# Optimization experiments

Measured on AMD Instinct MI355X. Metric: run time of the kernel, lower is better.

The kernel has to match this reference:

```python
import jax, jax.numpy as jnp
import numpy as np

B, T, N, F = 4, 12, 768, 32
H, K, KT, L = 64, 2, 3, 2
E = 24576
EPS = 1e-5


def setup_inputs() -> dict:
    key = jax.random.key(0)
    ks = iter(jax.random.split(key, 32))
    nrm = lambda shp, s=0.05: jax.random.normal(next(ks), shp, jnp.float32) * s
    inp = dict(
        x=jax.random.normal(next(ks), (B, T, N, F), jnp.float32),
        edge_index=jax.random.randint(next(ks), (2, E), 0, N),
        edge_weight=jax.random.uniform(next(ks), (E,), jnp.float32),
        in_proj_w=nrm((F, H)), in_proj_b=jnp.zeros((H,), jnp.float32),
        tc_w=nrm((L, 2, 3, H, H, KT)),           # [layer, tconv1/2, P/Q/R, out, in, k]
        tc_b=jnp.zeros((L, 2, 3, H), jnp.float32),
        cheb_w=nrm((L, K, H, H)), cheb_b=jnp.zeros((L, H), jnp.float32),
        bn_g=jnp.ones((L, N), jnp.float32), bn_b=jnp.zeros((L, N), jnp.float32),
        ln_g=jnp.ones((L, H), jnp.float32), ln_b=jnp.zeros((L, H), jnp.float32),
        out1_w=nrm((2 * H, H // 2)), out1_b=jnp.zeros((H // 2,), jnp.float32),
        oln_g=jnp.ones((H // 2,), jnp.float32), oln_b=jnp.zeros((H // 2,), jnp.float32),
        out2_w=nrm((H // 2, 1)), out2_b=jnp.zeros((1,), jnp.float32),
    )
    return inp


def _tconv(x, w, b):
    # gated temporal conv (GLU-style), 'same' padding along T. x: [B,T,N,C]
    xt = x.transpose(0, 3, 2, 1)  # [B,C,N,T]
    pad = (KT - 1) // 2
    def c(i):
        y = jax.lax.conv_general_dilated(
            xt, w[i][:, :, None, :], (1, 1), ((0, 0), (pad, pad)),
            dimension_numbers=('NCHW', 'OIHW', 'NCHW'))
        return y + b[i][None, :, None, None]
    out = jax.nn.relu(c(0) * jax.nn.sigmoid(c(1)) + c(2))
    return out.transpose(0, 3, 2, 1)


def _cheb(x, row, col, lap_w, theta, bias):
    # ChebConv with lambda_max=2: L_hat = -D^-1/2 A D^-1/2. x: [B,T,N,C]
    def lhat(z):
        zn = z.transpose(2, 0, 1, 3)                      # [N,B,T,C]
        msg = zn[col] * lap_w[:, None, None, None]        # gather source nodes
        agg = jax.ops.segment_sum(msg, row, num_segments=N)
        return agg.transpose(1, 2, 0, 3)
    tx0 = x
    out = jnp.einsum('btnc,cd->btnd', tx0, theta[0])
    if K > 1:
        tx1 = lhat(tx0)
        out = out + jnp.einsum('btnc,cd->btnd', tx1, theta[1])
        for k in range(2, K):
            tx2 = 2.0 * lhat(tx1) - tx0
            out = out + jnp.einsum('btnc,cd->btnd', tx2, theta[k])
            tx0, tx1 = tx1, tx2
    return out + bias


def reference(x, edge_index, edge_weight, in_proj_w, in_proj_b, tc_w, tc_b,
              cheb_w, cheb_b, bn_g, bn_b, ln_g, ln_b,
              out1_w, out1_b, oln_g, oln_b, out2_w, out2_b):
    row, col = edge_index[0], edge_index[1]
    deg = jax.ops.segment_sum(edge_weight, row, num_segments=N)
    dinv = jnp.where(deg > 0, jax.lax.rsqrt(jnp.maximum(deg, 1e-12)), 0.0)
    lap_w = -dinv[row] * edge_weight * dinv[col]

    h = x @ in_proj_w + in_proj_b  # [B,T,N,H]
    for l in range(L):
        z = _tconv(h, tc_w[l, 0], tc_b[l, 0])
        z = jax.nn.relu(_cheb(z, row, col, lap_w, cheb_w[l], cheb_b[l]))
        z = _tconv(z, tc_w[l, 1], tc_b[l, 1])
        # BatchNorm2d with nodes as channels: stats over (B,T,C) per node
        mu = z.mean(axis=(0, 1, 3), keepdims=True)
        var = z.var(axis=(0, 1, 3), keepdims=True)
        z = (z - mu) * jax.lax.rsqrt(var + EPS)
        z = z * bn_g[l][None, None, :, None] + bn_b[l][None, None, :, None]
        # LayerNorm over feature dim
        m2 = z.mean(-1, keepdims=True)
        v2 = z.var(-1, keepdims=True)
        z = (z - m2) * jax.lax.rsqrt(v2 + EPS) * ln_g[l] + ln_b[l]
        h = h + z  # dropout = identity (eval)

    emb = h[:, -1]  # [B,N,H] last timestep
    # pairwise linear: cat([row_h, col_h]) @ W == row_h @ W[:H] + col_h @ W[H:]
    a = emb @ out1_w[:H]             # [B,N,H/2]
    c = emb @ out1_w[H:] + out1_b    # [B,N,H/2]
    p = jax.nn.relu(a[:, :, None, :] + c[:, None, :, :])  # [B,N,N,H/2]
    pm = p.mean(-1, keepdims=True)
    pv = p.var(-1, keepdims=True)
    p = (p - pm) * jax.lax.rsqrt(pv + EPS) * oln_g + oln_b
    logits = (p @ out2_w)[..., 0] + out2_b[0]
    return jax.nn.sigmoid(logits)  # [B,N,N]
```

## Files before the change

kernel.cpp:

```cpp
#include <hip/hip_runtime.h>
#include <math.h>

#define NODES 768
#define BB 4
#define TT 12
#define FF 32
#define HH 64
#define EE 24576
#define EPSV 1e-5f

typedef short bf16x8 __attribute__((ext_vector_type(8)));
typedef float f32x4  __attribute__((ext_vector_type(4)));

__device__ __forceinline__ unsigned short f2bf(float f) {
  union { float f; unsigned int u; } c; c.f = f;
  unsigned int u = c.u;
  unsigned int r = (u + 0x7FFFu + ((u >> 16) & 1u)) >> 16;
  return (unsigned short)r;
}

constexpr int OFF_DEG    = 0;
constexpr int OFF_CNT    = 768;
constexpr int OFF_ROWPTR = 1600;
constexpr int OFF_OFF    = 2432;
constexpr int OFF_COLS   = 3200;
constexpr int OFF_WSEW   = 27776;
constexpr int OFF_WT     = 52352;
constexpr int OFF_THT    = 199808;
constexpr int OFF_WIN    = 216192;
constexpr int OFF_GW     = 222336;
constexpr int OFF_H      = 222400;
constexpr int OFF_ZA     = 2581696;
constexpr int OFF_ZB     = 4940992;
constexpr int OFF_AGG    = 7300288;
constexpr int OFF_MU     = 9659584;
constexpr int OFF_RSTD   = 9660352;
constexpr int OFF_A      = 9661120;
constexpr int OFF_C      = 9759424;

__global__ void prep_kernel(const float* __restrict__ tc_w, const float* __restrict__ cheb_w,
                            const float* __restrict__ in_proj_w, const float* __restrict__ out1_w,
                            const float* __restrict__ oln_g, const float* __restrict__ oln_b,
                            const float* __restrict__ out2_w, float* __restrict__ ws) {
  int idx = blockIdx.x * 256 + threadIdx.x;
  if (idx < 147456) {
    int lj = idx / 36864; int r = idx % 36864;
    int ks = r / 6144;    int r2 = r % 6144;
    int nt = r2 / 512;    int r3 = r2 % 512;
    int l  = r3 >> 3;     int j  = r3 & 7;
    int k  = ks * 32 + ((l >> 4) << 3) + j;
    int kk = k >> 6;      int in = k & 63;
    int col = nt * 16 + (l & 15);
    int g = col >> 6;     int o  = col & 63;
    float v = tc_w[(((lj * 3 + g) * 64 + o) * 64 + in) * 3 + kk];
    ((unsigned short*)(ws + OFF_WT))[idx] = f2bf(v);
  }
  int idx2 = idx - 147456;
  if (idx2 >= 0 && idx2 < 16384) {
    int i = idx2 & 63; int t = idx2 >> 6;
    int o = t & 63; t >>= 6;
    int k = t & 1; int l = t >> 1;
    ws[OFF_THT + idx2] = cheb_w[((l*2 + k)*64 + i)*64 + o];
  }
  int idx3 = idx2 - 16384;
  if (idx3 >= 0 && idx3 < 2048) {
    int i = idx3 & 31; int o = idx3 >> 5;
    ws[OFF_WIN + idx3] = in_proj_w[i*64 + o];
  }
  int idx5 = idx3 - 2048;
  if (idx5 >= 0 && idx5 < 768) {
    ws[OFF_DEG + idx5] = 0.0f;
    ((int*)ws)[OFF_CNT + idx5] = 0;
  }
  int idx6 = idx5 - 768;
  if (idx6 == 0) {
    float S1 = 0.f, S2 = 0.f;
    for (int d = 0; d < 32; d++) {
      float gw = oln_g[d] * out2_w[d];
      ws[OFF_GW + d] = gw;
      S1 += gw;
      S2 += oln_b[d] * out2_w[d];
    }
    ws[OFF_GW + 32] = S1;
    ws[OFF_GW + 33] = S2;
  }
}

__global__ void count_kernel(const int* __restrict__ edge_index, const float* __restrict__ ew,
                             float* __restrict__ ws) {
  int e = blockIdx.x * 256 + threadIdx.x;
  if (e >= EE) return;
  int r = edge_index[e];
  atomicAdd(&ws[OFF_DEG + r], ew[e]);
  atomicAdd(&((int*)ws)[OFF_CNT + r], 1);
}

__global__ void scan_kernel(float* __restrict__ ws) {
  __shared__ int s[NODES];
  int t = threadIdx.x;
  int* counts = (int*)ws + OFF_CNT;
  int* rowptr = (int*)ws + OFF_ROWPTR;
  int* off    = (int*)ws + OFF_OFF;
  int c = counts[t];
  s[t] = c;
  __syncthreads();
  for (int d = 1; d < NODES; d <<= 1) {
    int v = (t >= d) ? s[t - d] : 0;
    __syncthreads();
    s[t] += v;
    __syncthreads();
  }
  rowptr[t + 1] = s[t];
  if (t == 0) rowptr[0] = 0;
  off[t] = s[t] - c;
}

__global__ void scatter_kernel(const int* __restrict__ edge_index, const float* __restrict__ ew,
                               float* __restrict__ ws) {
  int e = blockIdx.x * 256 + threadIdx.x;
  if (e >= EE) return;
  int r = edge_index[e];
  int c = edge_index[EE + e];
  float w = ew[e];
  float dr = ws[OFF_DEG + r], dc = ws[OFF_DEG + c];
  float dir = dr > 0.f ? rsqrtf(fmaxf(dr, 1e-12f)) : 0.f;
  float dic = dc > 0.f ? rsqrtf(fmaxf(dc, 1e-12f)) : 0.f;
  float lw = -dir * w * dic;
  int pos = atomicAdd(&((int*)ws)[OFF_OFF + r], 1);
  ((int*)ws)[OFF_COLS + pos] = c;
  ws[OFF_WSEW + pos] = lw;
}

__global__ __launch_bounds__(64) void inproj_kernel(const float* __restrict__ x,
                                                    const float* __restrict__ in_proj_b,
                                                    float* __restrict__ ws) {
  int bid = blockIdx.x;
  int r0 = (bid >> 2) << 6;
  int o0 = (bid & 3) << 4;
  int row = r0 + threadIdx.x;
  float xr[32];
  const float4* xp = (const float4*)(x + row * 32);
#pragma unroll
  for (int i = 0; i < 8; i++) {
    float4 v = xp[i];
    xr[4*i] = v.x; xr[4*i+1] = v.y; xr[4*i+2] = v.z; xr[4*i+3] = v.w;
  }
  const float* WT = ws + OFF_WIN;
  float* h = ws + OFF_H;
  float4 res[4];
  float* rf = (float*)res;
#pragma unroll
  for (int oo = 0; oo < 16; oo++) {
    int o = o0 + oo;
    float acc = in_proj_b[o];
#pragma unroll
    for (int i = 0; i < 32; i++) acc += xr[i] * WT[o * 32 + i];
    rf[oo] = acc;
  }
  float4* op = (float4*)(h + row * 64 + o0);
#pragma unroll
  for (int q = 0; q < 4; q++) op[q] = res[q];
}

__global__ __launch_bounds__(256) void tconv_kernel(const float* __restrict__ src,
                                                    float* __restrict__ dst,
                                                    const unsigned short* __restrict__ WB,
                                                    const float* __restrict__ bias) {
  __shared__ unsigned short zls[6656];
  __shared__ float cbuf[12 * 192];
  unsigned char* zb = (unsigned char*)zls;
  int tid = threadIdx.x;
  int lane = tid & 63;
  int w = tid >> 6;
  int P0 = blockIdx.x * 6;
  int b  = P0 / NODES;
  int n0 = P0 % NODES;

  bf16x8 bfr[6][3];
#pragma unroll
  for (int ks = 0; ks < 6; ks++) {
#pragma unroll
    for (int c = 0; c < 3; c++) {
      int nt = w * 3 + c;
      bfr[ks][c] = *(const bf16x8*)(WB + (((ks * 12 + nt) * 64 + lane) << 3));
    }
  }
  float B0 = bias[tid & 63];
  float B1 = bias[64 + (tid & 63)];
  float B2 = bias[128 + (tid & 63)];

  for (int e = tid; e < 768; e += 256) {
    int pl = e / 128; int rr = (e >> 6) & 1; int in = e & 63;
    int ts = rr ? 13 : 0;
    int off = pl * 1792 + ts * 128 + ((in * 2) ^ ((ts & 7) << 4));
    *(unsigned short*)(zb + off) = 0;
  }
  for (int e = tid; e < 4608; e += 256) {
    int t = e / 384; int r = e % 384; int pl = r >> 6; int in = r & 63;
    float v = src[((b * TT + t) * NODES + n0 + pl) * HH + in];
    int ts = t + 1;
    int off = pl * 1792 + ts * 128 + ((in * 2) ^ ((ts & 7) << 4));
    *(unsigned short*)(zb + off) = f2bf(v);
  }
  __syncthreads();

  int tb = (lane >> 4) << 2;
  int cc = lane & 15;
  for (int p = 0; p < 6; p++) {
    bf16x8 afr[6];
#pragma unroll
    for (int ks = 0; ks < 6; ks++) {
      int k0 = ks * 32 + ((lane >> 4) << 3);
      int kk = k0 >> 6; int in0 = k0 & 63;
      int ts = (lane & 15) + kk;
      int off = p * 1792 + ts * 128 + ((in0 * 2) ^ ((ts & 7) << 4));
      afr[ks] = *(const bf16x8*)(zb + off);
    }
    f32x4 a0 = {0.f, 0.f, 0.f, 0.f};
    f32x4 a1 = a0, a2 = a0;
#pragma unroll
    for (int ks = 0; ks < 6; ks++) {
      a0 = __builtin_amdgcn_mfma_f32_16x16x32_bf16(afr[ks], bfr[ks][0], a0, 0, 0, 0);
      a1 = __builtin_amdgcn_mfma_f32_16x16x32_bf16(afr[ks], bfr[ks][1], a1, 0, 0, 0);
      a2 = __builtin_amdgcn_mfma_f32_16x16x32_bf16(afr[ks], bfr[ks][2], a2, 0, 0, 0);
    }
    __syncthreads();
#pragma unroll
    for (int r = 0; r < 4; r++) {
      int t = tb + r;
      if (t < 12) {
        cbuf[t * 192 + (w * 3 + 0) * 16 + cc] = a0[r];
        cbuf[t * 192 + (w * 3 + 1) * 16 + cc] = a1[r];
        cbuf[t * 192 + (w * 3 + 2) * 16 + cc] = a2[r];
      }
    }
    __syncthreads();
    int o = tid & 63;
    int n = n0 + p;
#pragma unroll
    for (int m = 0; m < 3; m++) {
      int t = (tid >> 6) + (m << 2);
      float v0 = cbuf[t * 192 + o]       + B0;
      float v1 = cbuf[t * 192 + 64 + o]  + B1;
      float v2 = cbuf[t * 192 + 128 + o] + B2;
      float g = 1.f / (1.f + __expf(-v1));
      dst[((b * TT + t) * NODES + n) * HH + o] = fmaxf(v0 * g + v2, 0.f);
    }
  }
}

__global__ __launch_bounds__(256) void agg_kernel(const float* __restrict__ za,
                                                  float* __restrict__ agg,
                                                  const float* __restrict__ ws) {
  int n = blockIdx.x >> 1;
  int half = blockIdx.x & 1;
  const int* rowptr = (const int*)ws + OFF_ROWPTR;
  const int* cols = (const int*)ws + OFF_COLS;
  const float* wsrt = ws + OFF_WSEW;
  int e0 = rowptr[n], e1 = rowptr[n + 1];
  int tid = threadIdx.x;
  int hh = tid & 63;
  int bt0 = tid >> 6;
  float acc[6];
#pragma unroll
  for (int p = 0; p < 6; p++) acc[p] = 0.f;
  for (int e = e0; e < e1; e++) {
    int c = cols[e];
    float w = wsrt[e];
    const float* zp = za + c * HH + hh;
#pragma unroll
    for (int p = 0; p < 6; p++) {
      int bt = bt0 + (((half * 6) + p) << 2);
      acc[p] += w * zp[bt * NODES * HH];
    }
  }
#pragma unroll
  for (int p = 0; p < 6; p++) {
    int bt = bt0 + (((half * 6) + p) << 2);
    agg[(bt * NODES + n) * HH + hh] = acc[p];
  }
}

__global__ __launch_bounds__(64) void cheb_kernel(const float* __restrict__ za,
                                                  const float* __restrict__ agg,
                                                  float* __restrict__ zb,
                                                  const float* __restrict__ thetaT,
                                                  const float* __restrict__ bias) {
  int bid = blockIdx.x;
  int r0 = (bid >> 2) << 6;
  int o0 = (bid & 3) << 4;
  int row = r0 + threadIdx.x;
  float xz[64], xa[64];
  const float4* zp = (const float4*)(za + row * 64);
  const float4* ap = (const float4*)(agg + row * 64);
#pragma unroll
  for (int i = 0; i < 16; i++) {
    float4 v = zp[i];
    xz[4*i] = v.x; xz[4*i+1] = v.y; xz[4*i+2] = v.z; xz[4*i+3] = v.w;
    float4 w = ap[i];
    xa[4*i] = w.x; xa[4*i+1] = w.y; xa[4*i+2] = w.z; xa[4*i+3] = w.w;
  }
  float4 res[4];
  float* rf = (float*)res;
#pragma unroll
  for (int oo = 0; oo < 16; oo++) {
    int o = o0 + oo;
    float acc = bias[o];
    const float* t0 = thetaT + o * 64;
    const float* t1 = thetaT + 4096 + o * 64;
#pragma unroll
    for (int i = 0; i < 64; i++) acc += xz[i] * t0[i] + xa[i] * t1[i];
    rf[oo] = fmaxf(acc, 0.f);
  }
  float4* op = (float4*)(zb + row * 64 + o0);
#pragma unroll
  for (int q = 0; q < 4; q++) op[q] = res[q];
}

__global__ __launch_bounds__(256) void bnstat_kernel(const float* __restrict__ z,
                                                     float* __restrict__ mu,
                                                     float* __restrict__ rstd) {
  int n = blockIdx.x;
  int tid = threadIdx.x;
  float s = 0.f, ss = 0.f;
  for (int p = tid; p < 48 * 64; p += 256) {
    int bt = p >> 6, hh = p & 63;
    float v = z[(bt * NODES + n) * HH + hh];
    s += v; ss += v * v;
  }
  int wave = tid >> 6, lane = tid & 63;
#pragma unroll
  for (int d = 32; d >= 1; d >>= 1) { s += __shfl_down(s, d, 64); ss += __shfl_down(ss, d, 64); }
  __shared__ float rs[4], rss[4];
  if (lane == 0) { rs[wave] = s; rss[wave] = ss; }
  __syncthreads();
  if (tid == 0) {
    float S = 0.f, SS = 0.f;
    for (int w = 0; w < 4; w++) { S += rs[w]; SS += rss[w]; }
    float m = S / 3072.f;
    float var = SS / 3072.f - m * m;
    mu[n] = m;
    rstd[n] = rsqrtf(var + EPSV);
  }
}

__global__ __launch_bounds__(256) void bnln_kernel(const float* __restrict__ z,
                                                   float* __restrict__ h,
                                                   const float* __restrict__ mu,
                                                   const float* __restrict__ rstd,
                                                   const float* __restrict__ bn_g,
                                                   const float* __restrict__ bn_b,
                                                   const float* __restrict__ ln_g,
                                                   const float* __restrict__ ln_b) {
  int row = blockIdx.x * 4 + (threadIdx.x >> 6);
  int lane = threadIdx.x & 63;
  int n = row % NODES;
  float v = z[row * 64 + lane];
  v = (v - mu[n]) * rstd[n] * bn_g[n] + bn_b[n];
  float s = v, ss = v * v;
#pragma unroll
  for (int d = 32; d >= 1; d >>= 1) { s += __shfl_xor(s, d, 64); ss += __shfl_xor(ss, d, 64); }
  float m = s * (1.f / 64.f);
  float var = ss * (1.f / 64.f) - m * m;
  float r2 = rsqrtf(var + EPSV);
  v = (v - m) * r2 * ln_g[lane] + ln_b[lane];
  h[row * 64 + lane] += v;
}

__global__ __launch_bounds__(256) void proj_kernel(const float* __restrict__ out1_w,
                                                   const float* __restrict__ out1_b,
                                                   float* __restrict__ ws) {
  __shared__ float wl[128 * 32];
  __shared__ float rl[4][64];
  int r0 = blockIdx.x * 4;
  int tid = threadIdx.x;
  const float* h = ws + OFF_H;
  for (int p = tid; p < 4096; p += 256) wl[p] = out1_w[p];
  {
    int rr = tid >> 6, ii = tid & 63;
    int row = r0 + rr;
    int b = row / NODES, n = row % NODES;
    rl[rr][ii] = h[((b * TT + (TT - 1)) * NODES + n) * 64 + ii];
  }
  __syncthreads();
  int rr = tid >> 6;
  int o = tid & 63;
  int part = o >> 5, oc = o & 31;
  float acc = part ? out1_b[oc] : 0.f;
  const float* wcol = wl + part * 64 * 32;
#pragma unroll
  for (int i = 0; i < 64; i++) acc += rl[rr][i] * wcol[i * 32 + oc];
  int row = r0 + rr;
  if (part == 0) (ws + OFF_A)[row * 32 + oc] = acc;
  else           (ws + OFF_C)[row * 32 + oc] = acc;
}

__global__ __launch_bounds__(256) void pair_kernel(const float* __restrict__ ws,
                                                   const float* __restrict__ out2_b,
                                                   float* __restrict__ out) {
  __shared__ float al[16 * 33], cl[16 * 33], gwl[34];
  int bidx = blockIdx.x;
  int b = bidx / (48 * 48);
  int rem = bidx % (48 * 48);
  int i0 = (rem / 48) * 16;
  int j0 = (rem % 48) * 16;
  int tid = threadIdx.x;
  const float* abuf = ws + OFF_A;
  const float* cbuf = ws + OFF_C;
  if (tid < 34) gwl[tid] = ws[OFF_GW + tid];
  for (int p = tid; p < 512; p += 256) {
    int rr = p >> 5, dd = p & 31;
    al[rr * 33 + dd] = abuf[(b * NODES + i0 + rr) * 32 + dd];
    cl[rr * 33 + dd] = cbuf[(b * NODES + j0 + rr) * 32 + dd];
  }
  __syncthreads();
  int ti = tid >> 4;
  int tj = tid & 15;
  float s1 = 0.f, s2 = 0.f, sg = 0.f;
#pragma unroll
  for (int d = 0; d < 32; d++) {
    float v = al[ti * 33 + d] + cl[tj * 33 + d];
    v = fmaxf(v, 0.f);
    s1 += v; s2 += v * v; sg += v * gwl[d];
  }
  float m = s1 * (1.f / 32.f);
  float var = s2 * (1.f / 32.f) - m * m;
  float rstd = rsqrtf(var + EPSV);
  float logit = rstd * (sg - m * gwl[32]) + gwl[33] + out2_b[0];
  float sig = 1.f / (1.f + __expf(-logit));
  out[(b * NODES + (i0 + ti)) * NODES + (j0 + tj)] = sig;
}

extern "C" void kernel_launch(void* const* d_in, const int* in_sizes, int n_in,
                              void* d_out, int out_size, void* d_ws, size_t ws_size,
                              hipStream_t stream) {
  const float* x          = (const float*)d_in[0];
  const int*   edge_index = (const int*)d_in[1];
  const float* edge_weight= (const float*)d_in[2];
  const float* in_proj_w  = (const float*)d_in[3];
  const float* in_proj_b  = (const float*)d_in[4];
  const float* tc_w       = (const float*)d_in[5];
  const float* tc_b       = (const float*)d_in[6];
  const float* cheb_w     = (const float*)d_in[7];
  const float* cheb_b     = (const float*)d_in[8];
  const float* bn_g       = (const float*)d_in[9];
  const float* bn_b       = (const float*)d_in[10];
  const float* ln_g       = (const float*)d_in[11];
  const float* ln_b       = (const float*)d_in[12];
  const float* out1_w     = (const float*)d_in[13];
  const float* out1_b     = (const float*)d_in[14];
  const float* oln_g      = (const float*)d_in[15];
  const float* oln_b      = (const float*)d_in[16];
  const float* out2_w     = (const float*)d_in[17];
  const float* out2_b     = (const float*)d_in[18];
  float* ws  = (float*)d_ws;
  float* out = (float*)d_out;

  hipLaunchKernelGGL(prep_kernel, dim3(668), dim3(256), 0, stream,
                     tc_w, cheb_w, in_proj_w, out1_w, oln_g, oln_b, out2_w, ws);
  hipLaunchKernelGGL(count_kernel, dim3(96), dim3(256), 0, stream, edge_index, edge_weight, ws);
  hipLaunchKernelGGL(scan_kernel, dim3(1), dim3(768), 0, stream, ws);
  hipLaunchKernelGGL(scatter_kernel, dim3(96), dim3(256), 0, stream, edge_index, edge_weight, ws);
  hipLaunchKernelGGL(inproj_kernel, dim3(2304), dim3(64), 0, stream, x, in_proj_b, ws);

  float* h   = ws + OFF_H;
  float* za  = ws + OFF_ZA;
  float* zb  = ws + OFF_ZB;
  float* agg = ws + OFF_AGG;
  float* mu  = ws + OFF_MU;
  float* rstd= ws + OFF_RSTD;
  const unsigned short* WB = (const unsigned short*)(ws + OFF_WT);

  for (int l = 0; l < 2; l++) {
    hipLaunchKernelGGL(tconv_kernel, dim3(512), dim3(256), 0, stream,
                       h, za, WB + (l * 2 + 0) * 36864, tc_b + (l * 2 + 0) * 192);
    hipLaunchKernelGGL(agg_kernel, dim3(1536), dim3(256), 0, stream, za, agg, ws);
    hipLaunchKernelGGL(cheb_kernel, dim3(2304), dim3(64), 0, stream,
                       za, agg, zb, ws + OFF_THT + l * 8192, cheb_b + l * 64);
    hipLaunchKernelGGL(tconv_kernel, dim3(512), dim3(256), 0, stream,
                       zb, za, WB + (l * 2 + 1) * 36864, tc_b + (l * 2 + 1) * 192);
    hipLaunchKernelGGL(bnstat_kernel, dim3(768), dim3(256), 0, stream, za, mu, rstd);
    hipLaunchKernelGGL(bnln_kernel, dim3(9216), dim3(256), 0, stream,
                       za, h, mu, rstd, bn_g + l * NODES, bn_b + l * NODES,
                       ln_g + l * 64, ln_b + l * 64);
  }

  hipLaunchKernelGGL(proj_kernel, dim3(768), dim3(256), 0, stream, out1_w, out1_b, ws);
  hipLaunchKernelGGL(pair_kernel, dim3(9216), dim3(256), 0, stream, ws, out2_b, out);
}
```

Baseline: 330.4 us.

## Fuse graph preprocessing, halve tconv tile, fuse batchnorm stats with layernorm

Merges the count, scan and scatter kernels into one single-block kernel that keeps degrees and offsets in shared memory, removing two launches and the global atomics. Halves the nodes per tconv block (6 to 3), doubling the grid to 1024 blocks, and switches to float4 loads with packed bf16 stores. Fuses the batchnorm statistics and the BN+LN apply into one per-node kernel that caches the node slice in LDS, removing a second pass over z. The single-block graph kernel serializes 24K edges on one CU, and smaller tconv tiles reload the weights more often.

```diff
diff --git a/kernel.cpp b/kernel.cpp
--- a/kernel.cpp
+++ b/kernel.cpp
@@ -19,10 +19,7 @@
   return (unsigned short)r;
 }
 
-constexpr int OFF_DEG    = 0;
-constexpr int OFF_CNT    = 768;
 constexpr int OFF_ROWPTR = 1600;
-constexpr int OFF_OFF    = 2432;
 constexpr int OFF_COLS   = 3200;
 constexpr int OFF_WSEW   = 27776;
 constexpr int OFF_WT     = 52352;
@@ -33,8 +30,6 @@
 constexpr int OFF_ZA     = 2581696;
 constexpr int OFF_ZB     = 4940992;
 constexpr int OFF_AGG    = 7300288;
-constexpr int OFF_MU     = 9659584;
-constexpr int OFF_RSTD   = 9660352;
 constexpr int OFF_A      = 9661120;
 constexpr int OFF_C      = 9759424;
 
@@ -67,12 +62,7 @@
     int i = idx3 & 31; int o = idx3 >> 5;
     ws[OFF_WIN + idx3] = in_proj_w[i*64 + o];
   }
-  int idx5 = idx3 - 2048;
-  if (idx5 >= 0 && idx5 < 768) {
-    ws[OFF_DEG + idx5] = 0.0f;
-    ((int*)ws)[OFF_CNT + idx5] = 0;
-  }
-  int idx6 = idx5 - 768;
+  int idx6 = idx3 - 2048;
   if (idx6 == 0) {
     float S1 = 0.f, S2 = 0.f;
     for (int d = 0; d < 32; d++) {
@@ -86,49 +76,50 @@
   }
 }
 
-__global__ void count_kernel(const int* __restrict__ edge_index, const float* __restrict__ ew,
-                             float* __restrict__ ws) {
-  int e = blockIdx.x * 256 + threadIdx.x;
-  if (e >= EE) return;
-  int r = edge_index[e];
-  atomicAdd(&ws[OFF_DEG + r], ew[e]);
-  atomicAdd(&((int*)ws)[OFF_CNT + r], 1);
-}
-
-__global__ void scan_kernel(float* __restrict__ ws) {
-  __shared__ int s[NODES];
-  int t = threadIdx.x;
-  int* counts = (int*)ws + OFF_CNT;
-  int* rowptr = (int*)ws + OFF_ROWPTR;
-  int* off    = (int*)ws + OFF_OFF;
-  int c = counts[t];
-  s[t] = c;
+__global__ __launch_bounds__(1024) void graph_kernel(const int* __restrict__ ei,
+                                                     const float* __restrict__ ew,
+                                                     float* __restrict__ ws) {
+  __shared__ float sdeg[NODES];
+  __shared__ int scnt[NODES];
+  __shared__ int soff[NODES];
+  __shared__ int sscan[NODES];
+  int tid = threadIdx.x;
+  if (tid < NODES) { sdeg[tid] = 0.f; scnt[tid] = 0; }
+  __syncthreads();
+  for (int e = tid; e < EE; e += 1024) {
+    int r = ei[e];
+    atomicAdd(&sdeg[r], ew[e]);
+    atomicAdd(&scnt[r], 1);
+  }
+  __syncthreads();
+  int c = (tid < NODES) ? scnt[tid] : 0;
+  if (tid < NODES) sscan[tid] = c;
   __syncthreads();
   for (int d = 1; d < NODES; d <<= 1) {
-    int v = (t >= d) ? s[t - d] : 0;
+    int v = 0;
+    if (tid < NODES && tid >= d) v = sscan[tid - d];
     __syncthreads();
-    s[t] += v;
+    if (tid < NODES) sscan[tid] += v;
     __syncthreads();
   }
-  rowptr[t + 1] = s[t];
-  if (t == 0) rowptr[0] = 0;
-  off[t] = s[t] - c;
-}
-
-__global__ void scatter_kernel(const int* __restrict__ edge_index, const float* __restrict__ ew,
-                               float* __restrict__ ws) {
-  int e = blockIdx.x * 256 + threadIdx.x;
-  if (e >= EE) return;
-  int r = edge_index[e];
-  int c = edge_index[EE + e];
-  float w = ew[e];
-  float dr = ws[OFF_DEG + r], dc = ws[OFF_DEG + c];
-  float dir = dr > 0.f ? rsqrtf(fmaxf(dr, 1e-12f)) : 0.f;
-  float dic = dc > 0.f ? rsqrtf(fmaxf(dc, 1e-12f)) : 0.f;
-  float lw = -dir * w * dic;
-  int pos = atomicAdd(&((int*)ws)[OFF_OFF + r], 1);
-  ((int*)ws)[OFF_COLS + pos] = c;
-  ws[OFF_WSEW + pos] = lw;
+  if (tid < NODES) {
+    soff[tid] = sscan[tid] - c;
+    ((int*)ws)[OFF_ROWPTR + tid + 1] = sscan[tid];
+    if (tid == 0) ((int*)ws)[OFF_ROWPTR] = 0;
+  }
+  __syncthreads();
+  for (int e = tid; e < EE; e += 1024) {
+    int r = ei[e];
+    int col = ei[EE + e];
+    float w = ew[e];
+    float dr = sdeg[r], dc = sdeg[col];
+    float dir = dr > 0.f ? rsqrtf(fmaxf(dr, 1e-12f)) : 0.f;
+    float dic = dc > 0.f ? rsqrtf(fmaxf(dc, 1e-12f)) : 0.f;
+    float lw = -dir * w * dic;
+    int pos = atomicAdd(&soff[r], 1);
+    ((int*)ws)[OFF_COLS + pos] = col;
+    ws[OFF_WSEW + pos] = lw;
+  }
 }
 
 __global__ __launch_bounds__(64) void inproj_kernel(const float* __restrict__ x,
@@ -166,13 +157,13 @@
                                                     float* __restrict__ dst,
                                                     const unsigned short* __restrict__ WB,
                                                     const float* __restrict__ bias) {
-  __shared__ unsigned short zls[6656];
+  __shared__ unsigned short zls[3072];
   __shared__ float cbuf[12 * 192];
   unsigned char* zb = (unsigned char*)zls;
   int tid = threadIdx.x;
   int lane = tid & 63;
   int w = tid >> 6;
-  int P0 = blockIdx.x * 6;
+  int P0 = blockIdx.x * 3;
   int b  = P0 / NODES;
   int n0 = P0 % NODES;
 
@@ -189,24 +180,28 @@
   float B1 = bias[64 + (tid & 63)];
   float B2 = bias[128 + (tid & 63)];
 
-  for (int e = tid; e < 768; e += 256) {
+  for (int e = tid; e < 384; e += 256) {
     int pl = e / 128; int rr = (e >> 6) & 1; int in = e & 63;
     int ts = rr ? 13 : 0;
     int off = pl * 1792 + ts * 128 + ((in * 2) ^ ((ts & 7) << 4));
     *(unsigned short*)(zb + off) = 0;
   }
-  for (int e = tid; e < 4608; e += 256) {
-    int t = e / 384; int r = e % 384; int pl = r >> 6; int in = r & 63;
-    float v = src[((b * TT + t) * NODES + n0 + pl) * HH + in];
+  for (int e = tid; e < 576; e += 256) {
+    int pl = e / 192; int rem = e % 192; int t = rem >> 4; int i4 = rem & 15;
+    int c0 = i4 << 2;
+    float4 v = *(const float4*)(src + ((b * TT + t) * NODES + n0 + pl) * HH + c0);
     int ts = t + 1;
-    int off = pl * 1792 + ts * 128 + ((in * 2) ^ ((ts & 7) << 4));
-    *(unsigned short*)(zb + off) = f2bf(v);
+    int base = pl * 1792 + ts * 128;
+    unsigned int lo = ((unsigned int)f2bf(v.y) << 16) | f2bf(v.x);
+    unsigned int hi = ((unsigned int)f2bf(v.w) << 16) | f2bf(v.z);
+    *(unsigned int*)(zb + (base + (((c0    ) * 2) ^ ((ts & 7) << 4)))) = lo;
+    *(unsigned int*)(zb + (base + (((c0 + 2) * 2) ^ ((ts & 7) << 4)))) = hi;
   }
   __syncthreads();
 
   int tb = (lane >> 4) << 2;
   int cc = lane & 15;
-  for (int p = 0; p < 6; p++) {
+  for (int p = 0; p < 3; p++) {
     bf16x8 afr[6];
 #pragma unroll
     for (int ks = 0; ks < 6; ks++) {
@@ -317,54 +312,53 @@
   for (int q = 0; q < 4; q++) op[q] = res[q];
 }
 
-__global__ __launch_bounds__(256) void bnstat_kernel(const float* __restrict__ z,
-                                                     float* __restrict__ mu,
-                                                     float* __restrict__ rstd) {
+__global__ __launch_bounds__(256) void bn_kernel(const float* __restrict__ z,
+                                                 float* __restrict__ h,
+                                                 const float* __restrict__ bn_g,
+                                                 const float* __restrict__ bn_b,
+                                                 const float* __restrict__ ln_g,
+                                                 const float* __restrict__ ln_b) {
+  __shared__ float zl[48 * 64];
+  __shared__ float rs[4], rss[4];
+  __shared__ float sstat[2];
   int n = blockIdx.x;
   int tid = threadIdx.x;
+  int wave = tid >> 6, lane = tid & 63;
   float s = 0.f, ss = 0.f;
-  for (int p = tid; p < 48 * 64; p += 256) {
+  for (int p = tid; p < 3072; p += 256) {
     int bt = p >> 6, hh = p & 63;
     float v = z[(bt * NODES + n) * HH + hh];
+    zl[p] = v;
     s += v; ss += v * v;
   }
-  int wave = tid >> 6, lane = tid & 63;
 #pragma unroll
   for (int d = 32; d >= 1; d >>= 1) { s += __shfl_down(s, d, 64); ss += __shfl_down(ss, d, 64); }
-  __shared__ float rs[4], rss[4];
   if (lane == 0) { rs[wave] = s; rss[wave] = ss; }
   __syncthreads();
   if (tid == 0) {
-    float S = 0.f, SS = 0.f;
-    for (int w = 0; w < 4; w++) { S += rs[w]; SS += rss[w]; }
+    float S = rs[0] + rs[1] + rs[2] + rs[3];
+    float SS = rss[0] + rss[1] + rss[2] + rss[3];
     float m = S / 3072.f;
     float var = SS / 3072.f - m * m;
-    mu[n] = m;
-    rstd[n] = rsqrtf(var + EPSV);
-  }
-}
-
-__global__ __launch_bounds__(256) void bnln_kernel(const float* __restrict__ z,
-                                                   float* __restrict__ h,
-                                                   const float* __restrict__ mu,
-                                                   const float* __restrict__ rstd,
-                                                   const float* __restrict__ bn_g,
-                                                   const float* __restrict__ bn_b,
-                                                   const float* __restrict__ ln_g,
-                                                   const float* __restrict__ ln_b) {
-  int row = blockIdx.x * 4 + (threadIdx.x >> 6);
-  int lane = threadIdx.x & 63;
-  int n = row % NODES;
-  float v = z[row * 64 + lane];
-  v = (v - mu[n]) * rstd[n] * bn_g[n] + bn_b[n];
-  float s = v, ss = v * v;
-#pragma unroll
-  for (int d = 32; d >= 1; d >>= 1) { s += __shfl_xor(s, d, 64); ss += __shfl_xor(ss, d, 64); }
-  float m = s * (1.f / 64.f);
-  float var = ss * (1.f / 64.f) - m * m;
-  float r2 = rsqrtf(var + EPSV);
-  v = (v - m) * r2 * ln_g[lane] + ln_b[lane];
-  h[row * 64 + lane] += v;
+    sstat[0] = m; sstat[1] = rsqrtf(var + EPSV);
+  }
+  __syncthreads();
+  float mu = sstat[0], rstd = sstat[1];
+  float bg = bn_g[n] * rstd;
+  float bbb = bn_b[n] - mu * bg;
+  float lg = ln_g[lane], lb = ln_b[lane];
+  for (int k = 0; k < 12; k++) {
+    int bt = wave + (k << 2);
+    float v = zl[bt * 64 + lane] * bg + bbb;
+    float s1 = v, s2 = v * v;
+#pragma unroll
+    for (int d = 32; d >= 1; d >>= 1) { s1 += __shfl_xor(s1, d, 64); s2 += __shfl_xor(s2, d, 64); }
+    float m = s1 * (1.f / 64.f);
+    float var = s2 * (1.f / 64.f) - m * m;
+    float r2 = rsqrtf(var + EPSV);
+    v = (v - m) * r2 * lg + lb;
+    h[(bt * NODES + n) * HH + lane] += v;
+  }
 }
 
 __global__ __launch_bounds__(256) void proj_kernel(const float* __restrict__ out1_w,
@@ -458,30 +452,25 @@
 
   hipLaunchKernelGGL(prep_kernel, dim3(668), dim3(256), 0, stream,
                      tc_w, cheb_w, in_proj_w, out1_w, oln_g, oln_b, out2_w, ws);
-  hipLaunchKernelGGL(count_kernel, dim3(96), dim3(256), 0, stream, edge_index, edge_weight, ws);
-  hipLaunchKernelGGL(scan_kernel, dim3(1), dim3(768), 0, stream, ws);
-  hipLaunchKernelGGL(scatter_kernel, dim3(96), dim3(256), 0, stream, edge_index, edge_weight, ws);
+  hipLaunchKernelGGL(graph_kernel, dim3(1), dim3(1024), 0, stream, edge_index, edge_weight, ws);
   hipLaunchKernelGGL(inproj_kernel, dim3(2304), dim3(64), 0, stream, x, in_proj_b, ws);
 
   float* h   = ws + OFF_H;
   float* za  = ws + OFF_ZA;
   float* zb  = ws + OFF_ZB;
   float* agg = ws + OFF_AGG;
-  float* mu  = ws + OFF_MU;
-  float* rstd= ws + OFF_RSTD;
   const unsigned short* WB = (const unsigned short*)(ws + OFF_WT);
 
   for (int l = 0; l < 2; l++) {
-    hipLaunchKernelGGL(tconv_kernel, dim3(512), dim3(256), 0, stream,
+    hipLaunchKernelGGL(tconv_kernel, dim3(1024), dim3(256), 0, stream,
                        h, za, WB + (l * 2 + 0) * 36864, tc_b + (l * 2 + 0) * 192);
     hipLaunchKernelGGL(agg_kernel, dim3(1536), dim3(256), 0, stream, za, agg, ws);
     hipLaunchKernelGGL(cheb_kernel, dim3(2304), dim3(64), 0, stream,
                        za, agg, zb, ws + OFF_THT + l * 8192, cheb_b + l * 64);
-    hipLaunchKernelGGL(tconv_kernel, dim3(512), dim3(256), 0, stream,
+    hipLaunchKernelGGL(tconv_kernel, dim3(1024), dim3(256), 0, stream,
                        zb, za, WB + (l * 2 + 1) * 36864, tc_b + (l * 2 + 1) * 192);
-    hipLaunchKernelGGL(bnstat_kernel, dim3(768), dim3(256), 0, stream, za, mu, rstd);
-    hipLaunchKernelGGL(bnln_kernel, dim3(9216), dim3(256), 0, stream,
-                       za, h, mu, rstd, bn_g + l * NODES, bn_b + l * NODES,
+    hipLaunchKernelGGL(bn_kernel, dim3(768), dim3(256), 0, stream,
+                       za, h, bn_g + l * NODES, bn_b + l * NODES,
                        ln_g + l * 64, ln_b + l * 64);
   }
 
```

Result: slower. 377.9 us (+14.4%).
